# Performance work log

Hardware: AMD Instinct MI355X
Metric: run time of the kernel (lower is better)

Reference implementation:

```python
import jax, jax.numpy as jnp
import numpy as np
from itertools import combinations

NUM_FIELDS = 32
INPUT_DIM = 64
BATCH = 4096
PAIRS = np.array(list(combinations(range(NUM_FIELDS), 2)), dtype=np.int32)  # [P, 2], P=496


def setup_inputs() -> dict:
    key = jax.random.key(0)
    k1, k2 = jax.random.split(key)
    x = jax.random.normal(k1, (BATCH, NUM_FIELDS, INPUT_DIM), dtype=jnp.float32)
    # One Linear(D, D, bias=False) weight per field pair (nn.Linear convention: y = x @ W.T)
    W = jax.random.normal(k2, (PAIRS.shape[0], INPUT_DIM, INPUT_DIM), dtype=jnp.float32) * 0.05
    return {"x": x, "W": W}


def reference(x, W) -> jnp.ndarray:
    # x: [B, F, D], W: [P, D, D] where P = C(F, 2)
    pi = jnp.asarray(PAIRS[:, 0])  # first field of each pair
    pj = jnp.asarray(PAIRS[:, 1])  # second field of each pair
    xi = x[:, pi, :]  # [B, P, D]
    xj = x[:, pj, :]  # [B, P, D]
    # Batched tiny GEMM: y_p = xi_p @ W_p.T  (nn.Linear semantics), fused with multiply
    proj = jnp.einsum('bpd,pod->bpo', xi, W)  # [B, P, D]
    return proj * xj  # concat over pairs == stacked pair dim -> [B, P, D]
```

## Files before the change

kernel.cpp:

```cpp
#include <hip/hip_runtime.h>

#define NBATCH 4096
#define NF     32
#define DIM    64
#define NPAIRS 496

#define MTILE  128
#define LDAP   72

typedef _Float16 half8 __attribute__((ext_vector_type(8)));
typedef _Float16 half4v __attribute__((ext_vector_type(4)));
typedef float    floatx4 __attribute__((ext_vector_type(4)));

__global__ __launch_bounds__(256, 4)
void bilinear_mfma(const float* __restrict__ x, const float* __restrict__ W,
                   float* __restrict__ out) {
    __shared__ _Float16 sW[DIM * LDAP];
    __shared__ _Float16 sA[MTILE * LDAP];

    const int tid  = threadIdx.x;
    const int lane = tid & 63;
    const int wv   = tid >> 6;
    const int lrow = lane & 15;
    const int quad = lane >> 4;

    const int p  = blockIdx.x % NPAIRS;
    const int bt = blockIdx.x / NPAIRS;
    const int b0 = bt * MTILE;

    int fi = 0, rem = p;
    while (rem >= NF - 1 - fi) { rem -= NF - 1 - fi; ++fi; }
    const int fj = fi + 1 + rem;

    const float* Wp = W + (size_t)p * (DIM * DIM);
    #pragma unroll
    for (int it = 0; it < 4; ++it) {
        int idx = tid + 256 * it;
        int o   = idx >> 4;
        int c4  = (idx & 15) << 2;
        const float4 v = *(const float4*)(Wp + o * DIM + c4);
        half4v hv;
        hv[0] = (_Float16)v.x; hv[1] = (_Float16)v.y;
        hv[2] = (_Float16)v.z; hv[3] = (_Float16)v.w;
        *(half4v*)(&sW[o * LDAP + c4]) = hv;
    }

    #pragma unroll
    for (int it = 0; it < 8; ++it) {
        int idx = tid + 256 * it;
        int r   = idx >> 4;
        int c4  = (idx & 15) << 2;
        const float4 v = *(const float4*)(x + ((size_t)(b0 + r) * NF + fi) * DIM + c4);
        half4v hv;
        hv[0] = (_Float16)v.x; hv[1] = (_Float16)v.y;
        hv[2] = (_Float16)v.z; hv[3] = (_Float16)v.w;
        *(half4v*)(&sA[r * LDAP + c4]) = hv;
    }
    __syncthreads();

    floatx4 acc[2][4] = {};
    #pragma unroll
    for (int ks = 0; ks < 2; ++ks) {
        half8 af[2], bf[4];
        #pragma unroll
        for (int mt = 0; mt < 2; ++mt)
            af[mt] = *(const half8*)(&sA[(wv * 32 + mt * 16 + lrow) * LDAP + ks * 32 + quad * 8]);
        #pragma unroll
        for (int nt = 0; nt < 4; ++nt)
            bf[nt] = *(const half8*)(&sW[(nt * 16 + lrow) * LDAP + ks * 32 + quad * 8]);
        #pragma unroll
        for (int mt = 0; mt < 2; ++mt)
            #pragma unroll
            for (int nt = 0; nt < 4; ++nt)
                acc[mt][nt] = __builtin_amdgcn_mfma_f32_16x16x32_f16(af[mt], bf[nt], acc[mt][nt], 0, 0, 0);
    }

    #pragma unroll
    for (int mt = 0; mt < 2; ++mt) {
        #pragma unroll
        for (int r = 0; r < 4; ++r) {
            const int row = wv * 32 + mt * 16 + quad * 4 + r;
            const size_t b = (size_t)(b0 + row);
            const float* xjrow = x + (b * NF + fj) * DIM;
            float* orow = out + b * (NPAIRS * DIM) + (size_t)p * DIM;
            #pragma unroll
            for (int nt = 0; nt < 4; ++nt) {
                const int col = nt * 16 + lrow;
                __builtin_nontemporal_store(acc[mt][nt][r] * xjrow[col], &orow[col]);
            }
        }
    }
}

extern "C" void kernel_launch(void* const* d_in, const int* in_sizes, int n_in,
                              void* d_out, int out_size, void* d_ws, size_t ws_size,
                              hipStream_t stream) {
    const float* x = (const float*)d_in[0];
    const float* W = (const float*)d_in[1];
    float* out = (float*)d_out;

    dim3 grid(NPAIRS * (NBATCH / MTILE));
    bilinear_mfma<<<grid, 256, 0, stream>>>(x, W, out);
}
```

Measured before the change: 602.7 us.

## Swap MFMA operands to load x directly into registers and store float4 outputs

Swaps the MFMA operand roles so W is the A operand and x rows are the B operand. The x tile is loaded straight from global memory into registers, which removes the shared-memory staging buffer. Each lane then holds four consecutive output columns for one batch row, so the epilogue can use 16-byte loads of xj and 16-byte nontemporal stores instead of scalar ones. The cost is that the global loads of x are less coalesced (per-lane row fetches), and the syncthreads still runs for the W tile.

```diff
diff --git a/kernel.cpp b/kernel.cpp
--- a/kernel.cpp
+++ b/kernel.cpp
@@ -8,7 +8,7 @@
 #define MTILE  128
 #define LDAP   72
 
-typedef _Float16 half8 __attribute__((ext_vector_type(8)));
+typedef _Float16 half8  __attribute__((ext_vector_type(8)));
 typedef _Float16 half4v __attribute__((ext_vector_type(4)));
 typedef float    floatx4 __attribute__((ext_vector_type(4)));
 
@@ -16,7 +16,6 @@
 void bilinear_mfma(const float* __restrict__ x, const float* __restrict__ W,
                    float* __restrict__ out) {
     __shared__ _Float16 sW[DIM * LDAP];
-    __shared__ _Float16 sA[MTILE * LDAP];
 
     const int tid  = threadIdx.x;
     const int lane = tid & 63;
@@ -38,56 +37,60 @@
         int idx = tid + 256 * it;
         int o   = idx >> 4;
         int c4  = (idx & 15) << 2;
-        const float4 v = *(const float4*)(Wp + o * DIM + c4);
+        const floatx4 v = *(const floatx4*)(Wp + o * DIM + c4);
         half4v hv;
-        hv[0] = (_Float16)v.x; hv[1] = (_Float16)v.y;
-        hv[2] = (_Float16)v.z; hv[3] = (_Float16)v.w;
+        hv[0] = (_Float16)v[0]; hv[1] = (_Float16)v[1];
+        hv[2] = (_Float16)v[2]; hv[3] = (_Float16)v[3];
         *(half4v*)(&sW[o * LDAP + c4]) = hv;
     }
 
+    half8 bx[2][2];
     #pragma unroll
-    for (int it = 0; it < 8; ++it) {
-        int idx = tid + 256 * it;
-        int r   = idx >> 4;
-        int c4  = (idx & 15) << 2;
-        const float4 v = *(const float4*)(x + ((size_t)(b0 + r) * NF + fi) * DIM + c4);
-        half4v hv;
-        hv[0] = (_Float16)v.x; hv[1] = (_Float16)v.y;
-        hv[2] = (_Float16)v.z; hv[3] = (_Float16)v.w;
-        *(half4v*)(&sA[r * LDAP + c4]) = hv;
+    for (int bt2 = 0; bt2 < 2; ++bt2) {
+        const int b = b0 + wv * 32 + bt2 * 16 + lrow;
+        const float* xrow = x + ((size_t)b * NF + fi) * DIM;
+        #pragma unroll
+        for (int ks = 0; ks < 2; ++ks) {
+            const floatx4 v0 = *(const floatx4*)(xrow + ks * 32 + quad * 8);
+            const floatx4 v1 = *(const floatx4*)(xrow + ks * 32 + quad * 8 + 4);
+            half8 h;
+            h[0] = (_Float16)v0[0]; h[1] = (_Float16)v0[1];
+            h[2] = (_Float16)v0[2]; h[3] = (_Float16)v0[3];
+            h[4] = (_Float16)v1[0]; h[5] = (_Float16)v1[1];
+            h[6] = (_Float16)v1[2]; h[7] = (_Float16)v1[3];
+            bx[bt2][ks] = h;
+        }
     }
     __syncthreads();
 
     floatx4 acc[2][4] = {};
     #pragma unroll
     for (int ks = 0; ks < 2; ++ks) {
-        half8 af[2], bf[4];
+        half8 aw[4];
         #pragma unroll
-        for (int mt = 0; mt < 2; ++mt)
-            af[mt] = *(const half8*)(&sA[(wv * 32 + mt * 16 + lrow) * LDAP + ks * 32 + quad * 8]);
+        for (int ot = 0; ot < 4; ++ot)
+            aw[ot] = *(const half8*)(&sW[(ot * 16 + lrow) * LDAP + ks * 32 + quad * 8]);
         #pragma unroll
-        for (int nt = 0; nt < 4; ++nt)
-            bf[nt] = *(const half8*)(&sW[(nt * 16 + lrow) * LDAP + ks * 32 + quad * 8]);
-        #pragma unroll
-        for (int mt = 0; mt < 2; ++mt)
+        for (int bt2 = 0; bt2 < 2; ++bt2)
             #pragma unroll
-            for (int nt = 0; nt < 4; ++nt)
-                acc[mt][nt] = __builtin_amdgcn_mfma_f32_16x16x32_f16(af[mt], bf[nt], acc[mt][nt], 0, 0, 0);
+            for (int ot = 0; ot < 4; ++ot)
+                acc[bt2][ot] = __builtin_amdgcn_mfma_f32_16x16x32_f16(aw[ot], bx[bt2][ks], acc[bt2][ot], 0, 0, 0);
     }
 
     #pragma unroll
-    for (int mt = 0; mt < 2; ++mt) {
+    for (int bt2 = 0; bt2 < 2; ++bt2) {
+        const size_t b = (size_t)(b0 + wv * 32 + bt2 * 16 + lrow);
+        const float* xjrow = x + (b * NF + fj) * DIM;
+        float* orow = out + b * (NPAIRS * DIM) + (size_t)p * DIM;
         #pragma unroll
-        for (int r = 0; r < 4; ++r) {
-            const int row = wv * 32 + mt * 16 + quad * 4 + r;
-            const size_t b = (size_t)(b0 + row);
-            const float* xjrow = x + (b * NF + fj) * DIM;
-            float* orow = out + b * (NPAIRS * DIM) + (size_t)p * DIM;
-            #pragma unroll
-            for (int nt = 0; nt < 4; ++nt) {
-                const int col = nt * 16 + lrow;
-                __builtin_nontemporal_store(acc[mt][nt][r] * xjrow[col], &orow[col]);
-            }
+        for (int ot = 0; ot < 4; ++ot) {
+            const int o4 = ot * 16 + quad * 4;
+            const floatx4 xj = *(const floatx4*)(xjrow + o4);
+            const floatx4 a = acc[bt2][ot];
+            floatx4 res;
+            res[0] = a[0] * xj[0]; res[1] = a[1] * xj[1];
+            res[2] = a[2] * xj[2]; res[3] = a[3] * xj[3];
+            __builtin_nontemporal_store(res, (floatx4*)(orow + o4));
         }
     }
 }
```

Result: slower. 632.4 us (+4.9%).
